# Performance work log

Hardware: AMD Instinct MI355X
Metric: run time of the kernel (lower is better)

## Reference

```python
import jax, jax.numpy as jnp
import numpy as np

B, S, H = 128, 8000, 64


def setup_inputs() -> dict:
    key = jax.random.key(0)
    ks = jax.random.split(key, 7)
    scale = 1.0 / np.sqrt(H)
    return {
        "x": jax.random.normal(ks[0], (B, S), dtype=jnp.float32),
        "W_ih": jax.random.normal(ks[1], (H, 1), dtype=jnp.float32) * scale,
        "b_ih": jax.random.normal(ks[2], (H,), dtype=jnp.float32) * scale,
        "W_hh": jax.random.normal(ks[3], (H, H), dtype=jnp.float32) * scale,
        "b_hh": jax.random.normal(ks[4], (H,), dtype=jnp.float32) * scale,
        "fc_w": jax.random.normal(ks[5], (2, H), dtype=jnp.float32) * scale,
        "fc_b": jax.random.normal(ks[6], (2,), dtype=jnp.float32) * scale,
    }


def reference(x, W_ih, b_ih, W_hh, b_hh, fc_w, fc_b):
    # x: [B, S] -> xt: [S, B, 1] (transpose(0,1).view(-1, B, 1))
    xt = x.astype(jnp.float32).T[:, :, None]
    batch = x.shape[0]
    hidden = W_hh.shape[0]
    # Precompute input projection for all steps: [S, B, H]
    xproj = xt @ W_ih.T + b_ih + b_hh
    h0 = jnp.zeros((batch, hidden), dtype=jnp.float32)  # default nn.RNN zero init

    def step(h, xp):
        h_new = jnp.tanh(xp + h @ W_hh.T)
        return h_new, h_new

    _, out = jax.lax.scan(step, h0, xproj)  # [S, B, H]
    # fc + sigmoid, then transpose(0,1): [B, S, 2]
    o = jax.nn.sigmoid(out @ fc_w.T + fc_b)  # [S, B, 2]
    selectivity = o[..., 0]  # [S, B]
    score = o[..., 1]        # [S, B]
    prediction = (score * selectivity).sum(axis=0) / selectivity.sum(axis=0)
    return prediction  # [B]
```

## Files before the change

kernel.cpp:

```cpp
#include <hip/hip_runtime.h>
#include <math.h>

#define BATCH 128
#define SLEN  8000
#define HID   64
#define CHUNK 64
#define NCHUNK (SLEN / CHUNK)
#define ROWSTRIDE 68

__device__ __forceinline__ float fast_exp2(float x) { return __builtin_amdgcn_exp2f(x); }
__device__ __forceinline__ float fast_rcp(float x)  { return __builtin_amdgcn_rcpf(x); }

__device__ __forceinline__ float bcast_lane(float v, int lane) {
    return __int_as_float(__builtin_amdgcn_readlane(__float_as_int(v), lane));
}

__device__ __forceinline__ float tanh_fast(float x) {
    float ax = fabsf(x);
    float z  = fminf(ax * 2.8853900817779268f, 30.0f);
    float e  = fast_exp2(z);
    float r  = (e - 1.0f) * fast_rcp(e + 1.0f);
    return x < 0.0f ? -r : r;
}

__device__ __forceinline__ float sigmoid_fast(float x) {
    float z = fminf(fmaxf(-x * 1.4426950408889634f, -60.0f), 60.0f);
    float e = fast_exp2(z);
    return fast_rcp(1.0f + e);
}


#define PK_RL(J0, J1, ACC, WPK)                                             \
    asm volatile("v_readlane_b32 s60, %1, " #J0 "\n\t"                      \
                 "v_readlane_b32 s61, %1, " #J1 "\n\t"                      \
                 "v_pk_fma_f32 %0, %2, s[60:61], %0"                        \
                 : "+v"(ACC) : "v"(h), "v"(WPK) : "s60", "s61")

#define PK_V(ACC, WPK, HPK)                                                 \
    asm volatile("v_pk_fma_f32 %0, %1, %2, %0"                              \
                 : "+v"(ACC) : "v"(WPK), "v"(HPK))

__global__ __launch_bounds__(64) void rnn_pkfma_kernel(
    const float* __restrict__ x,
    const float* __restrict__ W_ih,
    const float* __restrict__ b_ih,
    const float* __restrict__ W_hh,
    const float* __restrict__ b_hh,
    const float* __restrict__ fc_w,
    const float* __restrict__ fc_b,
    float* __restrict__ out)
{
    __shared__ float hbuf[CHUNK * ROWSTRIDE];

    const int lane = threadIdx.x;
    const int b    = blockIdx.x;
    const float* xrow = x + (size_t)b * SLEN;

    float2 wpk[16], wpkh[16];
    #pragma unroll
    for (int q = 0; q < 8; ++q) {
        float4 t = ((const float4*)(W_hh + lane * HID))[q];
        wpk[2*q]   = make_float2(t.x, t.y);
        wpk[2*q+1] = make_float2(t.z, t.w);
    }
    #pragma unroll
    for (int q = 0; q < 8; ++q) {
        float4 t = ((const float4*)(W_hh + lane * HID))[8 + q];
        wpkh[2*q]   = make_float2(t.x, t.y);
        wpkh[2*q+1] = make_float2(t.z, t.w);
    }
    const float wih  = W_ih[lane];
    const float bias = b_ih[lane] + b_hh[lane];
    const float fcb0 = fc_b[0], fcb1 = fc_b[1];

    float h = 0.0f;
    float num = 0.0f, den = 0.0f;

    hbuf[63 * ROWSTRIDE + lane] = 0.0f;

    float xv_next = xrow[lane];

    #pragma unroll 1
    for (int c = 0; c < NCHUNK; ++c) {
        float xcur = xv_next;
        int nidx = (c + 1 < NCHUNK) ? (c + 1) * CHUNK + lane : lane;
        xv_next = xrow[nidx];

        #pragma unroll 4
        for (int r = 0; r < CHUNK; ++r) {
            const float2* hp2 = (const float2*)(hbuf + ((r + 63) & 63) * ROWSTRIDE);
            float2 hh[16];
            #pragma unroll
            for (int q = 0; q < 16; ++q) hh[q] = hp2[16 + q];

            float xv = bcast_lane(xcur, r);

            float2 a01 = make_float2(fmaf(wih, xv, bias), 0.0f);
            float2 a23 = make_float2(0.0f, 0.0f);

            PK_RL( 0,  1, a01, wpk[0]);  PK_RL( 2,  3, a23, wpk[1]);
            PK_RL( 4,  5, a01, wpk[2]);  PK_RL( 6,  7, a23, wpk[3]);
            PK_RL( 8,  9, a01, wpk[4]);  PK_RL(10, 11, a23, wpk[5]);
            PK_RL(12, 13, a01, wpk[6]);  PK_RL(14, 15, a23, wpk[7]);
            PK_RL(16, 17, a01, wpk[8]);  PK_RL(18, 19, a23, wpk[9]);
            PK_RL(20, 21, a01, wpk[10]); PK_RL(22, 23, a23, wpk[11]);
            PK_RL(24, 25, a01, wpk[12]); PK_RL(26, 27, a23, wpk[13]);
            PK_RL(28, 29, a01, wpk[14]); PK_RL(30, 31, a23, wpk[15]);

            #pragma unroll
            for (int q = 0; q < 8; ++q) {
                PK_V(a01, wpkh[2*q],   hh[2*q]);
                PK_V(a23, wpkh[2*q+1], hh[2*q+1]);
            }

            float a = (a01.x + a01.y) + (a23.x + a23.y);
            h = tanh_fast(a);
            hbuf[r * ROWSTRIDE + lane] = h;
        }
        __syncthreads();

        {
            const float4* rp = (const float4*)(hbuf + lane * ROWSTRIDE);
            float d0 = 0.f, d1 = 0.f;
            #pragma unroll
            for (int q = 0; q < 16; ++q) {
                float4 hv = rp[q];
                float4 f0 = ((const float4*)fc_w)[q];
                float4 f1 = ((const float4*)(fc_w + HID))[q];
                d0 += hv.x * f0.x + hv.y * f0.y + hv.z * f0.z + hv.w * f0.w;
                d1 += hv.x * f1.x + hv.y * f1.y + hv.z * f1.z + hv.w * f1.w;
            }
            float sel = sigmoid_fast(d0 + fcb0);
            float sco = sigmoid_fast(d1 + fcb1);
            num = fmaf(sco, sel, num);
            den += sel;
        }
        __syncthreads();
    }

    #pragma unroll
    for (int off = 32; off > 0; off >>= 1) {
        num += __shfl_down(num, off);
        den += __shfl_down(den, off);
    }
    if (lane == 0) out[b] = num / den;
}

extern "C" void kernel_launch(void* const* d_in, const int* in_sizes, int n_in,
                              void* d_out, int out_size, void* d_ws, size_t ws_size,
                              hipStream_t stream) {
    const float* x    = (const float*)d_in[0];
    const float* W_ih = (const float*)d_in[1];
    const float* b_ih = (const float*)d_in[2];
    const float* W_hh = (const float*)d_in[3];
    const float* b_hh = (const float*)d_in[4];
    const float* fc_w = (const float*)d_in[5];
    const float* fc_b = (const float*)d_in[6];
    float* out = (float*)d_out;

    rnn_pkfma_kernel<<<BATCH, 64, 0, stream>>>(x, W_ih, b_ih, W_hh, b_hh,
                                               fc_w, fc_b, out);
}
```

Before: 1.845 ms.

## Interleave two batch recurrences per wavefront to hide serial-step latency

Each 64-thread block now advances two independent batch rows in lockstep. Each row has its own LDS hidden-state buffer and its own readlane scalar registers. The readlane/pk_fma chains, LDS loads and tanh of the two rows are interleaved so that one row's work can fill the latency stalls of the other. The grid shrinks to 64 blocks, so half as many CUs are busy and each wave issues roughly twice the instructions per timestep, which may outweigh the latency hiding.

```diff
diff --git a/kernel.cpp b/kernel.cpp
--- a/kernel.cpp
+++ b/kernel.cpp
@@ -29,18 +29,23 @@
     return fast_rcp(1.0f + e);
 }
 
-
-#define PK_RL(J0, J1, ACC, WPK)                                             \
+#define PK_RLA(J0, J1, ACC, WPK)                                            \
     asm volatile("v_readlane_b32 s60, %1, " #J0 "\n\t"                      \
                  "v_readlane_b32 s61, %1, " #J1 "\n\t"                      \
                  "v_pk_fma_f32 %0, %2, s[60:61], %0"                        \
-                 : "+v"(ACC) : "v"(h), "v"(WPK) : "s60", "s61")
+                 : "+v"(ACC) : "v"(hA), "v"(WPK) : "s60", "s61")
+
+#define PK_RLB(J0, J1, ACC, WPK)                                            \
+    asm volatile("v_readlane_b32 s62, %1, " #J0 "\n\t"                      \
+                 "v_readlane_b32 s63, %1, " #J1 "\n\t"                      \
+                 "v_pk_fma_f32 %0, %2, s[62:63], %0"                        \
+                 : "+v"(ACC) : "v"(hB), "v"(WPK) : "s62", "s63")
 
 #define PK_V(ACC, WPK, HPK)                                                 \
     asm volatile("v_pk_fma_f32 %0, %1, %2, %0"                              \
                  : "+v"(ACC) : "v"(WPK), "v"(HPK))
 
-__global__ __launch_bounds__(64) void rnn_pkfma_kernel(
+__global__ __launch_bounds__(64) void rnn_dual_kernel(
     const float* __restrict__ x,
     const float* __restrict__ W_ih,
     const float* __restrict__ b_ih,
@@ -50,11 +55,13 @@
     const float* __restrict__ fc_b,
     float* __restrict__ out)
 {
-    __shared__ float hbuf[CHUNK * ROWSTRIDE];
+    __shared__ float hbA[CHUNK * ROWSTRIDE];
+    __shared__ float hbB[CHUNK * ROWSTRIDE];
 
     const int lane = threadIdx.x;
     const int b    = blockIdx.x;
-    const float* xrow = x + (size_t)b * SLEN;
+    const float* xrowA = x + (size_t)(2 * b) * SLEN;
+    const float* xrowB = x + (size_t)(2 * b + 1) * SLEN;
 
     float2 wpk[16], wpkh[16];
     #pragma unroll
@@ -73,77 +80,118 @@
     const float bias = b_ih[lane] + b_hh[lane];
     const float fcb0 = fc_b[0], fcb1 = fc_b[1];
 
-    float h = 0.0f;
-    float num = 0.0f, den = 0.0f;
-
-    hbuf[63 * ROWSTRIDE + lane] = 0.0f;
-
-    float xv_next = xrow[lane];
+    float hA = 0.0f, hB = 0.0f;
+    float numA = 0.0f, denA = 0.0f;
+    float numB = 0.0f, denB = 0.0f;
+
+    hbA[63 * ROWSTRIDE + lane] = 0.0f;
+    hbB[63 * ROWSTRIDE + lane] = 0.0f;
+
+    float xv_nextA = xrowA[lane];
+    float xv_nextB = xrowB[lane];
 
     #pragma unroll 1
     for (int c = 0; c < NCHUNK; ++c) {
-        float xcur = xv_next;
+        float xcurA = xv_nextA;
+        float xcurB = xv_nextB;
         int nidx = (c + 1 < NCHUNK) ? (c + 1) * CHUNK + lane : lane;
-        xv_next = xrow[nidx];
-
-        #pragma unroll 4
+        xv_nextA = xrowA[nidx];
+        xv_nextB = xrowB[nidx];
+
+        #pragma unroll 2
         for (int r = 0; r < CHUNK; ++r) {
-            const float2* hp2 = (const float2*)(hbuf + ((r + 63) & 63) * ROWSTRIDE);
-            float2 hh[16];
-            #pragma unroll
-            for (int q = 0; q < 16; ++q) hh[q] = hp2[16 + q];
-
-            float xv = bcast_lane(xcur, r);
-
-            float2 a01 = make_float2(fmaf(wih, xv, bias), 0.0f);
-            float2 a23 = make_float2(0.0f, 0.0f);
-
-            PK_RL( 0,  1, a01, wpk[0]);  PK_RL( 2,  3, a23, wpk[1]);
-            PK_RL( 4,  5, a01, wpk[2]);  PK_RL( 6,  7, a23, wpk[3]);
-            PK_RL( 8,  9, a01, wpk[4]);  PK_RL(10, 11, a23, wpk[5]);
-            PK_RL(12, 13, a01, wpk[6]);  PK_RL(14, 15, a23, wpk[7]);
-            PK_RL(16, 17, a01, wpk[8]);  PK_RL(18, 19, a23, wpk[9]);
-            PK_RL(20, 21, a01, wpk[10]); PK_RL(22, 23, a23, wpk[11]);
-            PK_RL(24, 25, a01, wpk[12]); PK_RL(26, 27, a23, wpk[13]);
-            PK_RL(28, 29, a01, wpk[14]); PK_RL(30, 31, a23, wpk[15]);
+            const float2* hpA = (const float2*)(hbA + ((r + 63) & 63) * ROWSTRIDE);
+            const float2* hpB = (const float2*)(hbB + ((r + 63) & 63) * ROWSTRIDE);
+            float2 hhA[16], hhB[16];
+            #pragma unroll
+            for (int q = 0; q < 16; ++q) hhA[q] = hpA[16 + q];
+            #pragma unroll
+            for (int q = 0; q < 16; ++q) hhB[q] = hpB[16 + q];
+
+            float xvA = bcast_lane(xcurA, r);
+            float xvB = bcast_lane(xcurB, r);
+
+            float2 a01A = make_float2(fmaf(wih, xvA, bias), 0.0f);
+            float2 a23A = make_float2(0.0f, 0.0f);
+            float2 a01B = make_float2(fmaf(wih, xvB, bias), 0.0f);
+            float2 a23B = make_float2(0.0f, 0.0f);
+
+            PK_RLA( 0,  1, a01A, wpk[0]);  PK_RLB( 0,  1, a01B, wpk[0]);
+            PK_RLA( 2,  3, a23A, wpk[1]);  PK_RLB( 2,  3, a23B, wpk[1]);
+            PK_RLA( 4,  5, a01A, wpk[2]);  PK_RLB( 4,  5, a01B, wpk[2]);
+            PK_RLA( 6,  7, a23A, wpk[3]);  PK_RLB( 6,  7, a23B, wpk[3]);
+            PK_RLA( 8,  9, a01A, wpk[4]);  PK_RLB( 8,  9, a01B, wpk[4]);
+            PK_RLA(10, 11, a23A, wpk[5]);  PK_RLB(10, 11, a23B, wpk[5]);
+            PK_RLA(12, 13, a01A, wpk[6]);  PK_RLB(12, 13, a01B, wpk[6]);
+            PK_RLA(14, 15, a23A, wpk[7]);  PK_RLB(14, 15, a23B, wpk[7]);
+            PK_RLA(16, 17, a01A, wpk[8]);  PK_RLB(16, 17, a01B, wpk[8]);
+            PK_RLA(18, 19, a23A, wpk[9]);  PK_RLB(18, 19, a23B, wpk[9]);
+            PK_RLA(20, 21, a01A, wpk[10]); PK_RLB(20, 21, a01B, wpk[10]);
+            PK_RLA(22, 23, a23A, wpk[11]); PK_RLB(22, 23, a23B, wpk[11]);
+            PK_RLA(24, 25, a01A, wpk[12]); PK_RLB(24, 25, a01B, wpk[12]);
+            PK_RLA(26, 27, a23A, wpk[13]); PK_RLB(26, 27, a23B, wpk[13]);
+            PK_RLA(28, 29, a01A, wpk[14]); PK_RLB(28, 29, a01B, wpk[14]);
+            PK_RLA(30, 31, a23A, wpk[15]); PK_RLB(30, 31, a23B, wpk[15]);
 
             #pragma unroll
             for (int q = 0; q < 8; ++q) {
-                PK_V(a01, wpkh[2*q],   hh[2*q]);
-                PK_V(a23, wpkh[2*q+1], hh[2*q+1]);
+                PK_V(a01A, wpkh[2*q],   hhA[2*q]);
+                PK_V(a23A, wpkh[2*q+1], hhA[2*q+1]);
             }
-
-            float a = (a01.x + a01.y) + (a23.x + a23.y);
-            h = tanh_fast(a);
-            hbuf[r * ROWSTRIDE + lane] = h;
+            #pragma unroll
+            for (int q = 0; q < 8; ++q) {
+                PK_V(a01B, wpkh[2*q],   hhB[2*q]);
+                PK_V(a23B, wpkh[2*q+1], hhB[2*q+1]);
+            }
+
+            float aA = (a01A.x + a01A.y) + (a23A.x + a23A.y);
+            hA = tanh_fast(aA);
+            hbA[r * ROWSTRIDE + lane] = hA;
+
+            float aB = (a01B.x + a01B.y) + (a23B.x + a23B.y);
+            hB = tanh_fast(aB);
+            hbB[r * ROWSTRIDE + lane] = hB;
         }
         __syncthreads();
 
         {
-            const float4* rp = (const float4*)(hbuf + lane * ROWSTRIDE);
-            float d0 = 0.f, d1 = 0.f;
+            const float4* rpA = (const float4*)(hbA + lane * ROWSTRIDE);
+            const float4* rpB = (const float4*)(hbB + lane * ROWSTRIDE);
+            float d0A = 0.f, d1A = 0.f, d0B = 0.f, d1B = 0.f;
             #pragma unroll
             for (int q = 0; q < 16; ++q) {
-                float4 hv = rp[q];
+                float4 hvA = rpA[q];
+                float4 hvB = rpB[q];
                 float4 f0 = ((const float4*)fc_w)[q];
                 float4 f1 = ((const float4*)(fc_w + HID))[q];
-                d0 += hv.x * f0.x + hv.y * f0.y + hv.z * f0.z + hv.w * f0.w;
-                d1 += hv.x * f1.x + hv.y * f1.y + hv.z * f1.z + hv.w * f1.w;
+                d0A += hvA.x * f0.x + hvA.y * f0.y + hvA.z * f0.z + hvA.w * f0.w;
+                d1A += hvA.x * f1.x + hvA.y * f1.y + hvA.z * f1.z + hvA.w * f1.w;
+                d0B += hvB.x * f0.x + hvB.y * f0.y + hvB.z * f0.z + hvB.w * f0.w;
+                d1B += hvB.x * f1.x + hvB.y * f1.y + hvB.z * f1.z + hvB.w * f1.w;
             }
-            float sel = sigmoid_fast(d0 + fcb0);
-            float sco = sigmoid_fast(d1 + fcb1);
-            num = fmaf(sco, sel, num);
-            den += sel;
+            float selA = sigmoid_fast(d0A + fcb0);
+            float scoA = sigmoid_fast(d1A + fcb1);
+            numA = fmaf(scoA, selA, numA);
+            denA += selA;
+            float selB = sigmoid_fast(d0B + fcb0);
+            float scoB = sigmoid_fast(d1B + fcb1);
+            numB = fmaf(scoB, selB, numB);
+            denB += selB;
         }
         __syncthreads();
     }
 
     #pragma unroll
     for (int off = 32; off > 0; off >>= 1) {
-        num += __shfl_down(num, off);
-        den += __shfl_down(den, off);
-    }
-    if (lane == 0) out[b] = num / den;
+        numA += __shfl_down(numA, off);
+        denA += __shfl_down(denA, off);
+        numB += __shfl_down(numB, off);
+        denB += __shfl_down(denB, off);
+    }
+    if (lane == 0) {
+        out[2 * b]     = numA / denA;
+        out[2 * b + 1] = numB / denB;
+    }
 }
 
 extern "C" void kernel_launch(void* const* d_in, const int* in_sizes, int n_in,
@@ -158,6 +206,6 @@
     const float* fc_b = (const float*)d_in[6];
     float* out = (float*)d_out;
 
-    rnn_pkfma_kernel<<<BATCH, 64, 0, stream>>>(x, W_ih, b_ih, W_hh, b_hh,
-                                               fc_w, fc_b, out);
-}
+    rnn_dual_kernel<<<BATCH / 2, 64, 0, stream>>>(x, W_ih, b_ih, W_hh, b_hh,
+                                                  fc_w, fc_b, out);
+}
```

Result: slower. 3.420 ms (+85.4%).
